# Kernel optimization log

Measured on AMD Instinct MI355X. Metric: run time of the kernel, lower is better.

The kernel has to match this reference:

```python
import jax, jax.numpy as jnp
import numpy as np

B, M, D, H, DH = 8, 1024, 768, 12, 64
R, RF, RW, DFF = 32, 384, 384, 3072
EPS = 1e-12  # BERT LayerNorm eps


def _ln(z, g, b):
    mu = jnp.mean(z, -1, keepdims=True)
    var = jnp.mean((z - mu) ** 2, -1, keepdims=True)
    return g * (z - mu) * jax.lax.rsqrt(var + EPS) + b


def setup_inputs() -> dict:
    ks = jax.random.split(jax.random.key(0), 20)
    n = lambda k, s: jax.random.normal(k, s, dtype=jnp.float32) * 0.02
    return {
        "x": jax.random.normal(ks[0], (B, M, D), dtype=jnp.float32),
        "mask": jnp.zeros((B, M), jnp.float32),  # additive attention mask
        "Pq": n(ks[1], (H, D, R)), "Vq": n(ks[2], (H, R, DH)), "bq": n(ks[3], (H, DH)),
        "Pk": n(ks[4], (H, D, R)), "Vk": n(ks[5], (H, R, DH)), "bk": n(ks[6], (H, DH)),
        "Pv": n(ks[7], (H, D, R)), "Vv": n(ks[8], (H, R, DH)), "bv": n(ks[9], (H, DH)),
        "Uo": n(ks[10], (D, RW)), "Vo": n(ks[11], (RW, D)), "bo_attn": n(ks[12], (D,)),
        "U1": n(ks[13], (D, RF)), "V1": n(ks[14], (RF, DFF)), "b1": n(ks[15], (DFF,)),
        "U2": n(ks[16], (DFF, RF)), "V2": n(ks[17], (RF, D)), "b2": n(ks[18], (D,)),
        "ln1_g": jnp.ones((D,), jnp.float32), "ln1_b": jnp.zeros((D,), jnp.float32),
        "ln2_g": jnp.ones((D,), jnp.float32), "ln2_b": jnp.zeros((D,), jnp.float32),
    }


def reference(x, mask, Pq, Vq, bq, Pk, Vk, bk, Pv, Vv, bv, Uo, Vo, bo_attn,
              U1, V1, b1, U2, V2, b2, ln1_g, ln1_b, ln2_g, ln2_b):
    Bx, Mx, dm = x.shape
    dh = dm // Pq.shape[0]
    scale = 1.0 / (dh ** 0.5)
    # low-rank per-head Q/K/V: x @ P (d->r) then @ V (r->dh), + per-head bias
    Q = jnp.einsum('bmd,hdr,hrk->bhmk', x, Pq, Vq) + bq[None, :, None, :]
    K = jnp.einsum('bmd,hdr,hrk->bhmk', x, Pk, Vk) + bk[None, :, None, :]
    V = jnp.einsum('bmd,hdr,hrk->bhmk', x, Pv, Vv) + bv[None, :, None, :]
    scores = jnp.einsum('bhmk,bhnk->bhmn', Q, K) * scale + mask[:, None, None, :]
    probs = jax.nn.softmax(scores, axis=-1)
    attn = jnp.einsum('bhmn,bhnk->bhmk', probs, V)
    attn = attn.transpose(0, 2, 1, 3).reshape(Bx, Mx, dm)  # (B, M, d_model)
    # low-rank attention output projection + residual + LN1
    x1 = _ln(x + (attn @ Uo) @ Vo + bo_attn, ln1_g, ln1_b)
    # low-rank FFN: GELU((x1 @ U1) @ V1 + b1) @ U2 @ V2 + b2 (BERT exact gelu)
    mid = x1 @ U1
    y = (jax.nn.gelu(mid @ V1 + b1, approximate=False) @ U2) @ V2 + b2
    return _ln(x1 + y, ln2_g, ln2_b)
```

## Files before the change

### kernel.cpp

```cpp
#include <hip/hip_runtime.h>
#include <cstddef>

#define D_MODEL 768
#define NHEAD   12
#define DHEAD   64
#define RANK    32
#define SEQ     1024
#define BATCH   8
#define BM      8192

typedef __attribute__((ext_vector_type(8))) short short8;
typedef __attribute__((ext_vector_type(4))) float floatx4;

__device__ inline ushort f2b(float f) {
  union { float f; unsigned u; } v; v.f = f;
  unsigned r = v.u + 0x7fffu + ((v.u >> 16) & 1u);
  return (ushort)(r >> 16);
}
__device__ inline float b2f(ushort h) {
  union { unsigned u; float f; } v; v.u = ((unsigned)h) << 16;
  return v.f;
}
__device__ inline unsigned pk2(float a, float b) {
  return ((__float_as_uint(b) + 0x8000u) & 0xffff0000u) |
         ((__float_as_uint(a) + 0x8000u) >> 16);
}
__device__ inline float fast_gelu(float x) {
  float z = 0.79788456080286536f * (x + 0.044715f * x * x * x);
  float e = __expf(2.f * z);
  float t = 1.f - 2.f / (e + 1.f);
  return 0.5f * x * (1.f + t);
}

__global__ __launch_bounds__(256) void f2b_kernel(
    const float* __restrict__ in, ushort* __restrict__ out, int n) {
  int i = (blockIdx.x * 256 + threadIdx.x) * 4;
  if (i >= n) return;
  float4 v = *(const float4*)(in + i);
  ushort4 o;
  o.x = f2b(v.x); o.y = f2b(v.y); o.z = f2b(v.z); o.w = f2b(v.w);
  *(ushort4*)(out + i) = o;
}

__global__ __launch_bounds__(256) void combine_qkv_kernel(
    const float* __restrict__ Pq, const float* __restrict__ Vq,
    const float* __restrict__ Pk, const float* __restrict__ Vk,
    const float* __restrict__ Pv, const float* __restrict__ Vv,
    ushort* __restrict__ Wt) {
  int which = blockIdx.y;
  const float* P  = which == 0 ? Pq : (which == 1 ? Pk : Pv);
  const float* Vw = which == 0 ? Vq : (which == 1 ? Vk : Vv);
  ushort* W = Wt + (size_t)which * D_MODEL * D_MODEL;
  int idx = blockIdx.x * 256 + threadIdx.x;
  if (idx >= D_MODEL * NHEAD * DHEAD) return;
  int c = idx / D_MODEL;
  int d = idx - c * D_MODEL;
  int h = c >> 6, k = c & 63;
  const float* p = P + ((size_t)h * D_MODEL + d) * RANK;
  const float* v = Vw + (size_t)h * RANK * DHEAD + k;
  float s = 0.f;
#pragma unroll
  for (int r = 0; r < RANK; r++) s += p[r] * v[(size_t)r * DHEAD];
  W[(size_t)c * D_MODEL + d] = f2b(s);
}

__global__ __launch_bounds__(256) void concat_bias_kernel(
    const float* __restrict__ bq, const float* __restrict__ bk,
    const float* __restrict__ bv, float* __restrict__ out) {
  int i = blockIdx.x * 256 + threadIdx.x;
  if (i >= 2304) return;
  out[i] = (i < 768) ? bq[i] : (i < 1536 ? bk[i - 768] : bv[i - 1536]);
}

__global__ __launch_bounds__(256) void prep_weights_kernel(
    const float* __restrict__ U1, const float* __restrict__ V1,
    const float* __restrict__ U2, const float* __restrict__ V2,
    const float* __restrict__ Vo, const float* __restrict__ Uo,
    ushort* __restrict__ U1t, ushort* __restrict__ V1t,
    ushort* __restrict__ U2t, ushort* __restrict__ V2t,
    ushort* __restrict__ VoT, ushort* __restrict__ Uob) {
  __shared__ float t[32][33];
  int blk = blockIdx.x;
  if (blk >= 3168) {
    int i = (blk - 3168) * 1024 + threadIdx.x * 4;
    float4 v = *(const float4*)(Uo + i);
    ushort4 o;
    o.x = f2b(v.x); o.y = f2b(v.y); o.z = f2b(v.z); o.w = f2b(v.w);
    *(ushort4*)(Uob + i) = o;
    return;
  }
  const float* in; ushort* out; int R, C, bx, by;
  if (blk < 288)       { in = U1; out = U1t; R = 768;  C = 384;  int i = blk;        bx = i % 12; by = i / 12; }
  else if (blk < 1440) { in = V1; out = V1t; R = 384;  C = 3072; int i = blk - 288;  bx = i % 96; by = i / 96; }
  else if (blk < 2592) { in = U2; out = U2t; R = 3072; C = 384;  int i = blk - 1440; bx = i % 12; by = i / 12; }
  else if (blk < 2880) { in = V2; out = V2t; R = 384;  C = 768;  int i = blk - 2592; bx = i % 24; by = i / 24; }
  else                 { in = Vo; out = VoT; R = 384;  C = 768;  int i = blk - 2880; bx = i % 24; by = i / 24; }
  int c0 = bx * 32, r0 = by * 32;
  int lx = threadIdx.x & 31, ly = threadIdx.x >> 5;
#pragma unroll
  for (int i = 0; i < 32; i += 8)
    t[ly + i][lx] = in[(size_t)(r0 + ly + i) * C + c0 + lx];
  __syncthreads();
#pragma unroll
  for (int i = 0; i < 32; i += 8)
    out[(size_t)(c0 + ly + i) * R + r0 + lx] = f2b(t[lx][ly + i]);
}

template <int OUTMODE, int BIAS, int GELU>
__global__ __launch_bounds__(256) void gemm_mfma_kernel(
    const ushort* __restrict__ A, const ushort* __restrict__ Bt,
    const float* __restrict__ bias, void* __restrict__ C,
    void* __restrict__ C2, void* __restrict__ C3,
    int M, int N, int K) {
  __shared__ __align__(16) ushort Als[128 * 32];
  __shared__ __align__(16) ushort Bls[128 * 32];
  const int tid  = threadIdx.x;
  const int lane = tid & 63;
  const int quad = lane >> 4, l16 = lane & 15;
  const int wu   = __builtin_amdgcn_readfirstlane(tid >> 6);
  const int wrow = (wu >> 1) * 64, wcol = (wu & 1) * 64;
  const int row0 = blockIdx.y * 128, col0 = blockIdx.x * 128;

  floatx4 acc[4][4] = {};

  for (int k0 = 0; k0 < K; k0 += 32) {
    __syncthreads();
#pragma unroll
    for (int is = 0; is < 2; is++) {
      int c = is * 256 + wu * 64 + lane;
      int m = c >> 2, kk = (c & 3) << 3;
      const ushort* ga = A + (size_t)(row0 + m) * K + (k0 + kk);
      ushort* la = Als + (size_t)(is * 256 + wu * 64) * 8;
      __builtin_amdgcn_global_load_lds(
          (const __attribute__((address_space(1))) void*)ga,
          (__attribute__((address_space(3))) void*)la, 16, 0, 0);
      const ushort* gb = Bt + (size_t)(col0 + m) * K + (k0 + kk);
      ushort* lb = Bls + (size_t)(is * 256 + wu * 64) * 8;
      __builtin_amdgcn_global_load_lds(
          (const __attribute__((address_space(1))) void*)gb,
          (__attribute__((address_space(3))) void*)lb, 16, 0, 0);
    }
    __syncthreads();

    short8 af[4], bf[4];
#pragma unroll
    for (int mt = 0; mt < 4; mt++)
      af[mt] = *(const short8*)(Als + ((wrow + mt * 16 + l16) * 32 + quad * 8));
#pragma unroll
    for (int nt = 0; nt < 4; nt++)
      bf[nt] = *(const short8*)(Bls + ((wcol + nt * 16 + l16) * 32 + quad * 8));
#pragma unroll
    for (int mt = 0; mt < 4; mt++)
#pragma unroll
      for (int nt = 0; nt < 4; nt++)
        acc[mt][nt] = __builtin_amdgcn_mfma_f32_16x16x32_bf16(
            af[mt], bf[nt], acc[mt][nt], 0, 0, 0);
  }

#pragma unroll
  for (int mt = 0; mt < 4; mt++) {
#pragma unroll
    for (int nt = 0; nt < 4; nt++) {
      int colg = col0 + wcol + nt * 16 + l16;
      float bv_ = BIAS ? bias[colg] : 0.f;
      float v4[4];
#pragma unroll
      for (int r = 0; r < 4; r++) {
        float v = acc[mt][nt][r] + bv_;
        if (GELU) v = fast_gelu(v);
        v4[r] = v;
      }
      int rowg0 = row0 + wrow + mt * 16 + quad * 4;
      if (OUTMODE == 3) {
        int seg = col0 / 768;
        int cl = colg - seg * 768;
        if (seg == 2) {
          ushort4 o;
          o.x = f2b(v4[0]); o.y = f2b(v4[1]); o.z = f2b(v4[2]); o.w = f2b(v4[3]);
          *(ushort4*)((ushort*)C3 + (size_t)cl * BM + rowg0) = o;
        } else {
          ushort* dst = (seg == 0) ? (ushort*)C : (ushort*)C2;
          float sc = (seg == 0) ? 0.125f : 1.f;
#pragma unroll
          for (int r = 0; r < 4; r++)
            dst[(size_t)(rowg0 + r) * D_MODEL + cl] = f2b(v4[r] * sc);
        }
      } else {
#pragma unroll
        for (int r = 0; r < 4; r++)
          ((ushort*)C)[(size_t)(rowg0 + r) * N + colg] = f2b(v4[r]);
      }
    }
  }
}

template <int BIAS>
__global__ __launch_bounds__(256) void gemm_n64_kernel(
    const ushort* __restrict__ A, const ushort* __restrict__ Bt,
    const float* __restrict__ bias, ushort* __restrict__ C,
    int M, int N, int K) {
  __shared__ __align__(16) ushort Als[128 * 32];
  __shared__ __align__(16) ushort Bls[64 * 32];
  const int tid  = threadIdx.x;
  const int lane = tid & 63;
  const int quad = lane >> 4, l16 = lane & 15;
  const int wu   = __builtin_amdgcn_readfirstlane(tid >> 6);
  const int row0 = blockIdx.y * 128, col0 = blockIdx.x * 64;

  floatx4 acc[2][4] = {};

  for (int k0 = 0; k0 < K; k0 += 32) {
    __syncthreads();
#pragma unroll
    for (int is = 0; is < 2; is++) {
      int c = is * 256 + wu * 64 + lane;
      int m = c >> 2, kk = (c & 3) << 3;
      const ushort* ga = A + (size_t)(row0 + m) * K + (k0 + kk);
      ushort* la = Als + (size_t)(is * 256 + wu * 64) * 8;
      __builtin_amdgcn_global_load_lds(
          (const __attribute__((address_space(1))) void*)ga,
          (__attribute__((address_space(3))) void*)la, 16, 0, 0);
    }
    {
      int c = wu * 64 + lane;
      int m = c >> 2, kk = (c & 3) << 3;
      const ushort* gb = Bt + (size_t)(col0 + m) * K + (k0 + kk);
      ushort* lb = Bls + (size_t)(wu * 64) * 8;
      __builtin_amdgcn_global_load_lds(
          (const __attribute__((address_space(1))) void*)gb,
          (__attribute__((address_space(3))) void*)lb, 16, 0, 0);
    }
    __syncthreads();

    short8 af[2], bf[4];
#pragma unroll
    for (int mt = 0; mt < 2; mt++)
      af[mt] = *(const short8*)(Als + ((wu * 32 + mt * 16 + l16) * 32 + quad * 8));
#pragma unroll
    for (int nt = 0; nt < 4; nt++)
      bf[nt] = *(const short8*)(Bls + ((nt * 16 + l16) * 32 + quad * 8));
#pragma unroll
    for (int mt = 0; mt < 2; mt++)
#pragma unroll
      for (int nt = 0; nt < 4; nt++)
        acc[mt][nt] = __builtin_amdgcn_mfma_f32_16x16x32_bf16(
            af[mt], bf[nt], acc[mt][nt], 0, 0, 0);
  }

#pragma unroll
  for (int mt = 0; mt < 2; mt++) {
#pragma unroll
    for (int nt = 0; nt < 4; nt++) {
      int colg = col0 + nt * 16 + l16;
      float bv_ = BIAS ? bias[colg] : 0.f;
      int rowg0 = row0 + wu * 32 + mt * 16 + quad * 4;
#pragma unroll
      for (int r = 0; r < 4; r++)
        C[(size_t)(rowg0 + r) * N + colg] = f2b(acc[mt][nt][r] + bv_);
    }
  }
}

__global__ __launch_bounds__(256) void gemm_mfma_splitk_kernel(
    const ushort* __restrict__ A, const ushort* __restrict__ Bt,
    float* __restrict__ Cpart, int M, int N, int Ktot, int Kper) {
  __shared__ __align__(16) ushort Als[128 * 32];
  __shared__ __align__(16) ushort Bls[128 * 32];
  const int tid  = threadIdx.x;
  const int lane = tid & 63;
  const int quad = lane >> 4, l16 = lane & 15;
  const int wu   = __builtin_amdgcn_readfirstlane(tid >> 6);
  const int wrow = (wu >> 1) * 64, wcol = (wu & 1) * 64;
  const int row0 = blockIdx.y * 128, col0 = blockIdx.x * 128;
  const int kbase = blockIdx.z * Kper;
  float* Cz = Cpart + (size_t)blockIdx.z * M * N;

  floatx4 acc[4][4] = {};

  for (int k0 = kbase; k0 < kbase + Kper; k0 += 32) {
    __syncthreads();
#pragma unroll
    for (int is = 0; is < 2; is++) {
      int c = is * 256 + wu * 64 + lane;
      int m = c >> 2, kk = (c & 3) << 3;
      const ushort* ga = A + (size_t)(row0 + m) * Ktot + (k0 + kk);
      ushort* la = Als + (size_t)(is * 256 + wu * 64) * 8;
      __builtin_amdgcn_global_load_lds(
          (const __attribute__((address_space(1))) void*)ga,
          (__attribute__((address_space(3))) void*)la, 16, 0, 0);
      const ushort* gb = Bt + (size_t)(col0 + m) * Ktot + (k0 + kk);
      ushort* lb = Bls + (size_t)(is * 256 + wu * 64) * 8;
      __builtin_amdgcn_global_load_lds(
          (const __attribute__((address_space(1))) void*)gb,
          (__attribute__((address_space(3))) void*)lb, 16, 0, 0);
    }
    __syncthreads();

    short8 af[4], bf[4];
#pragma unroll
    for (int mt = 0; mt < 4; mt++)
      af[mt] = *(const short8*)(Als + ((wrow + mt * 16 + l16) * 32 + quad * 8));
#pragma unroll
    for (int nt = 0; nt < 4; nt++)
      bf[nt] = *(const short8*)(Bls + ((wcol + nt * 16 + l16) * 32 + quad * 8));
#pragma unroll
    for (int mt = 0; mt < 4; mt++)
#pragma unroll
      for (int nt = 0; nt < 4; nt++)
        acc[mt][nt] = __builtin_amdgcn_mfma_f32_16x16x32_bf16(
            af[mt], bf[nt], acc[mt][nt], 0, 0, 0);
  }

#pragma unroll
  for (int mt = 0; mt < 4; mt++)
#pragma unroll
    for (int nt = 0; nt < 4; nt++) {
      int colg = col0 + wcol + nt * 16 + l16;
      int rowg0 = row0 + wrow + mt * 16 + quad * 4;
#pragma unroll
      for (int r = 0; r < 4; r++)
        Cz[(size_t)(rowg0 + r) * N + colg] = acc[mt][nt][r];
    }
}

__global__ __launch_bounds__(256) void reduce_splitk_kernel(
    const float* __restrict__ part, ushort* __restrict__ out, int n, int S) {
  int i = (blockIdx.x * 256 + threadIdx.x) * 4;
  if (i >= n) return;
  float4 a = *(const float4*)(part + i);
  for (int s = 1; s < S; s++) {
    float4 b = *(const float4*)(part + (size_t)s * n + i);
    a.x += b.x; a.y += b.y; a.z += b.z; a.w += b.w;
  }
  ushort4 o;
  o.x = f2b(a.x); o.y = f2b(a.y); o.z = f2b(a.z); o.w = f2b(a.w);
  *(ushort4*)(out + i) = o;
}

__global__ __launch_bounds__(256, 3) void attn_mfma_kernel(
    const ushort* __restrict__ Q, const ushort* __restrict__ K,
    const ushort* __restrict__ Vt, const float* __restrict__ mask,
    ushort* __restrict__ O) {
  const int bid  = blockIdx.x;
  const int xcd  = bid & 7;
  const int rest = bid >> 3;
  const int qt   = rest & 7;
  const int grp  = (rest >> 3) * 8 + xcd;
  const int h = grp % 12, b = grp / 12;

  const int tid = threadIdx.x;
  const int lane = tid & 63;
  const int quad = lane >> 4, l16 = lane & 15;
  const int wu = __builtin_amdgcn_readfirstlane(tid >> 6);
  const int qrow0 = qt * 128 + wu * 32;

  __shared__ __align__(16) ushort Ks[128 * 64];
  __shared__ __align__(16) ushort Vts[64 * 128];
  __shared__ __align__(16) float Msk[SEQ];

  *(float4*)(Msk + tid * 4) = *(const float4*)(mask + (size_t)b * SEQ + tid * 4);

  short8 qf[2][2];
#pragma unroll
  for (int rt = 0; rt < 2; rt++) {
    const ushort* qp = Q + ((size_t)(b * SEQ + qrow0 + rt * 16 + l16)) * D_MODEL
                     + h * DHEAD + quad * 8;
    qf[rt][0] = *(const short8*)qp;
    qf[rt][1] = *(const short8*)(qp + 32);
  }

  const int j0 = tid >> 3, ck = tid & 7;
  const int d0 = tid >> 4, cv = tid & 15;
  const ushort* Kg = K + ((size_t)(b * SEQ + j0)) * D_MODEL + h * DHEAD + ck * 8;
  const ushort* Vg = Vt + ((size_t)(h * DHEAD + d0)) * BM + b * SEQ + cv * 8;
  ushort* Kl = Ks + j0 * 64 + ((ck ^ (j0 & 7)) << 3);
  ushort* Vl = Vts + d0 * 128 + ((cv ^ (d0 & 15)) << 3);

  short8 kst[4], vst[4];
#pragma unroll
  for (int p = 0; p < 4; p++)
    kst[p] = *(const short8*)(Kg + (size_t)p * (32 * D_MODEL));
#pragma unroll
  for (int p = 0; p < 4; p++)
    vst[p] = *(const short8*)(Vg + (size_t)p * (16 * BM));

  float lsum[2] = {0.f, 0.f};
  floatx4 o_acc[2][4] = {};

  for (int n0 = 0; n0 < SEQ; n0 += 128) {
    asm volatile("" ::: "memory");
    __builtin_amdgcn_s_barrier();
    asm volatile("" ::: "memory");

#pragma unroll
    for (int p = 0; p < 4; p++) *(short8*)(Kl + p * (32 * 64)) = kst[p];
#pragma unroll
    for (int p = 0; p < 4; p++) *(short8*)(Vl + p * (16 * 128)) = vst[p];

    if (n0 + 128 < SEQ) {
#pragma unroll
      for (int p = 0; p < 4; p++)
        kst[p] = *(const short8*)(Kg + (size_t)(n0 + 128) * D_MODEL
                                     + (size_t)p * (32 * D_MODEL));
#pragma unroll
      for (int p = 0; p < 4; p++)
        vst[p] = *(const short8*)(Vg + (n0 + 128) + (size_t)p * (16 * BM));
    }

    asm volatile("s_waitcnt lgkmcnt(0)" ::: "memory");
    __builtin_amdgcn_s_barrier();
    asm volatile("" ::: "memory");

    unsigned UA[2][8], UB[2][8];
#pragma unroll
    for (int ct = 0; ct < 8; ct++) {
      int krow = ct * 16 + l16;
      int sa = (quad ^ (l16 & 7)) << 3;
      const ushort* kbp = Ks + krow * 64;
      short8 ka = *(const short8*)(kbp + sa);
      short8 kb = *(const short8*)(kbp + (sa ^ 32));
      float4 mk = *(const float4*)(Msk + n0 + ct * 16 + quad * 4);
#pragma unroll
      for (int rt = 0; rt < 2; rt++) {
        floatx4 st = {};
        st = __builtin_amdgcn_mfma_f32_16x16x32_bf16(ka, qf[rt][0], st, 0, 0, 0);
        st = __builtin_amdgcn_mfma_f32_16x16x32_bf16(kb, qf[rt][1], st, 0, 0, 0);
        float e0 = __expf(st[0] + mk.x);
        float e1 = __expf(st[1] + mk.y);
        float e2 = __expf(st[2] + mk.z);
        float e3 = __expf(st[3] + mk.w);
        lsum[rt] += (e0 + e1) + (e2 + e3);
        UA[rt][ct] = pk2(e0, e1);
        UB[rt][ct] = pk2(e2, e3);
      }
    }

#pragma unroll
    for (int kk = 0; kk < 4; kk++) {
      short8 pa[2];
#pragma unroll
      for (int rt = 0; rt < 2; rt++) {
        unsigned a0 = UA[rt][2 * kk], a2 = UA[rt][2 * kk + 1];
        unsigned b1 = UB[rt][2 * kk], b3 = UB[rt][2 * kk + 1];
        asm("v_permlane32_swap_b32 %0, %1" : "+v"(a0), "+v"(a2));
        asm("v_permlane16_swap_b32 %0, %1" : "+v"(a0), "+v"(a2));
        asm("v_permlane32_swap_b32 %0, %1" : "+v"(b1), "+v"(b3));
        asm("v_permlane16_swap_b32 %0, %1" : "+v"(b1), "+v"(b3));
        int4 t;
        t.x = (int)a0;
        t.y = (int)b1;
        t.z = (int)a2;
        t.w = (int)b3;
        pa[rt] = *(short8*)&t;
      }
#pragma unroll
      for (int dt = 0; dt < 4; dt++) {
        int vrow = dt * 16 + l16;
        short8 vb = *(const short8*)(Vts + vrow * 128
                                     + ((((kk * 4 + quad) ^ l16)) << 3));
#pragma unroll
        for (int rt = 0; rt < 2; rt++)
          o_acc[rt][dt] = __builtin_amdgcn_mfma_f32_16x16x32_bf16(pa[rt], vb, o_acc[rt][dt], 0, 0, 0);
      }
    }
  }

#pragma unroll
  for (int rt = 0; rt < 2; rt++) {
    float l = lsum[rt];
    l += __shfl_xor(l, 16);
    l += __shfl_xor(l, 32);
    float inv = 1.f / l;
    int lanebase = lane & 48;
#pragma unroll
    for (int rr = 0; rr < 4; rr++) {
      int iv = __builtin_amdgcn_ds_bpermute((lanebase | (quad * 4 + rr)) << 2,
                                            __float_as_int(inv));
      float invr = __int_as_float(iv);
      size_t rowg = (size_t)(b * SEQ + qrow0 + rt * 16 + quad * 4 + rr);
#pragma unroll
      for (int dt = 0; dt < 4; dt++)
        O[rowg * D_MODEL + h * DHEAD + dt * 16 + l16] = f2b(o_acc[rt][dt][rr] * invr);
    }
  }
}

template <int AIN_BF16, int OUT_FP32, int OUT_BF16>
__global__ __launch_bounds__(256) void add_ln_kernel(
    const float* __restrict__ Ainf, const ushort* __restrict__ Ainb,
    const ushort* __restrict__ Binb,
    const float* __restrict__ g, const float* __restrict__ bt,
    float* __restrict__ outf, ushort* __restrict__ outb) {
  const int row = blockIdx.x, tid = threadIdx.x;
  __shared__ float red[4];
  float v[3];
  float s = 0.f;
#pragma unroll
  for (int u = 0; u < 3; u++) {
    int c = tid + u * 256;
    float a = AIN_BF16 ? b2f(Ainb[(size_t)row * 768 + c]) : Ainf[(size_t)row * 768 + c];
    v[u] = a + b2f(Binb[(size_t)row * 768 + c]);
    s += v[u];
  }
#pragma unroll
  for (int off = 32; off > 0; off >>= 1) s += __shfl_down(s, off);
  if ((tid & 63) == 0) red[tid >> 6] = s;
  __syncthreads();
  float mu = (red[0] + red[1] + red[2] + red[3]) * (1.f / 768.f);
  float s2 = 0.f;
#pragma unroll
  for (int u = 0; u < 3; u++) { float d = v[u] - mu; s2 += d * d; }
#pragma unroll
  for (int off = 32; off > 0; off >>= 1) s2 += __shfl_down(s2, off);
  __syncthreads();
  if ((tid & 63) == 0) red[tid >> 6] = s2;
  __syncthreads();
  float var = (red[0] + red[1] + red[2] + red[3]) * (1.f / 768.f);
  float inv = rsqrtf(var + 1e-12f);
#pragma unroll
  for (int u = 0; u < 3; u++) {
    int c = tid + u * 256;
    float r = g[c] * (v[u] - mu) * inv + bt[c];
    if (OUT_FP32) outf[(size_t)row * 768 + c] = r;
    if (OUT_BF16) outb[(size_t)row * 768 + c] = f2b(r);
  }
}

extern "C" void kernel_launch(void* const* d_in, const int* in_sizes, int n_in,
                              void* d_out, int out_size, void* d_ws, size_t ws_size,
                              hipStream_t stream) {
  const float* x    = (const float*)d_in[0];
  const float* mask = (const float*)d_in[1];
  const float* Pq   = (const float*)d_in[2];
  const float* Vq   = (const float*)d_in[3];
  const float* bq   = (const float*)d_in[4];
  const float* Pk   = (const float*)d_in[5];
  const float* Vk   = (const float*)d_in[6];
  const float* bk   = (const float*)d_in[7];
  const float* Pv   = (const float*)d_in[8];
  const float* Vv   = (const float*)d_in[9];
  const float* bv   = (const float*)d_in[10];
  const float* Uo   = (const float*)d_in[11];
  const float* Vo   = (const float*)d_in[12];
  const float* bo   = (const float*)d_in[13];
  const float* U1   = (const float*)d_in[14];
  const float* V1   = (const float*)d_in[15];
  const float* b1   = (const float*)d_in[16];
  const float* U2   = (const float*)d_in[17];
  const float* V2   = (const float*)d_in[18];
  const float* b2   = (const float*)d_in[19];
  const float* g1   = (const float*)d_in[20];
  const float* be1  = (const float*)d_in[21];
  const float* g2   = (const float*)d_in[22];
  const float* be2  = (const float*)d_in[23];

  char* w = (char*)d_ws;
  auto alloc = [&](size_t bytes) -> char* {
    char* p = w; w += (bytes + 255) & ~(size_t)255; return p;
  };
  ushort* xb     = (ushort*)alloc((size_t)BM * 768 * 2);
  ushort* Wqkvt  = (ushort*)alloc((size_t)2304 * 768 * 2);
  float*  ball   = (float*)alloc(2304 * 4);
  ushort* VoT    = (ushort*)alloc(768 * 384 * 2);
  ushort* Uob    = (ushort*)alloc(768 * 384 * 2);
  ushort* Wot    = (ushort*)alloc(768 * 768 * 2);
  ushort* U1t    = (ushort*)alloc(384 * 768 * 2);
  ushort* V1t    = (ushort*)alloc((size_t)3072 * 384 * 2);
  ushort* U2t    = (ushort*)alloc((size_t)384 * 3072 * 2);
  ushort* V2t    = (ushort*)alloc(768 * 384 * 2);
  ushort* Qb     = (ushort*)alloc((size_t)BM * 768 * 2);
  ushort* Kb     = (ushort*)alloc((size_t)BM * 768 * 2);
  ushort* Vtb    = (ushort*)alloc((size_t)768 * BM * 2);
  ushort* attnb  = (ushort*)alloc((size_t)BM * 768 * 2);
  ushort* mtb    = (ushort*)alloc((size_t)BM * 384 * 2);
  ushort* y1b    = (ushort*)alloc((size_t)BM * 768 * 2);
  ushort* x1b    = (ushort*)alloc((size_t)BM * 768 * 2);
  float*  part   = (float*)alloc((size_t)4 * BM * 384 * 4);
  ushort* hiddenb = Qb;
  ushort* y2b     = y1b;
  float*  outp    = (float*)d_out;

  f2b_kernel<<<(BM * 768) / 1024, 256, 0, stream>>>(x, xb, BM * 768);
  combine_qkv_kernel<<<dim3(2304, 3), 256, 0, stream>>>(Pq, Vq, Pk, Vk, Pv, Vv, Wqkvt);
  concat_bias_kernel<<<9, 256, 0, stream>>>(bq, bk, bv, ball);
  prep_weights_kernel<<<3456, 256, 0, stream>>>(U1, V1, U2, V2, Vo, Uo,
                                                U1t, V1t, U2t, V2t, VoT, Uob);
  gemm_n64_kernel<0><<<dim3(12, 6), 256, 0, stream>>>(VoT, Uob, nullptr, Wot, 768, 768, 384);

  gemm_mfma_kernel<3, 1, 0><<<dim3(18, 64), 256, 0, stream>>>(
      xb, Wqkvt, ball, Qb, Kb, Vtb, BM, 2304, 768);

  attn_mfma_kernel<<<dim3(768), 256, 0, stream>>>(Qb, Kb, Vtb, mask, attnb);

  gemm_n64_kernel<1><<<dim3(12, 64), 256, 0, stream>>>(attnb, Wot, bo, y1b, BM, 768, 768);
  add_ln_kernel<0, 0, 1><<<BM, 256, 0, stream>>>(x, nullptr, y1b, g1, be1, nullptr, x1b);

  gemm_mfma_splitk_kernel<<<dim3(3, 64, 4), 256, 0, stream>>>(
      x1b, U1t, part, BM, 384, 768, 192);
  reduce_splitk_kernel<<<(BM * 384) / 1024, 256, 0, stream>>>(part, mtb, BM * 384, 4);
  gemm_mfma_kernel<1, 1, 1><<<dim3(24, 64), 256, 0, stream>>>(
      mtb, V1t, b1, hiddenb, nullptr, nullptr, BM, 3072, 384);
  gemm_mfma_splitk_kernel<<<dim3(3, 64, 4), 256, 0, stream>>>(
      hiddenb, U2t, part, BM, 384, 3072, 768);
  reduce_splitk_kernel<<<(BM * 384) / 1024, 256, 0, stream>>>(part, mtb, BM * 384, 4);
  gemm_n64_kernel<1><<<dim3(12, 64), 256, 0, stream>>>(mtb, V2t, b2, y2b, BM, 768, 384);

  add_ln_kernel<1, 1, 0><<<BM, 256, 0, stream>>>(nullptr, x1b, y2b, g2, be2, outp, nullptr);
}
```

Measured before the change: 461.0 us.

## Halve attention tile sizes to double grid and raise occupancy

The attention kernel now gives each block 64 query rows instead of 128, so each wave handles 16 rows, and streams K/V in 64-key chunks instead of 128. The grid doubles to 1536 blocks and launch bounds rise to 6 blocks per CU. Per-wave registers and LDS shrink, so more waves can hide latency. In exchange, K/V tiles are reloaded twice as often per query row, and there are more barriers per key processed.

```diff
diff --git a/kernel.cpp b/kernel.cpp
--- a/kernel.cpp
+++ b/kernel.cpp
@@ -337,137 +337,124 @@
   *(ushort4*)(out + i) = o;
 }
 
-__global__ __launch_bounds__(256, 3) void attn_mfma_kernel(
+__global__ __launch_bounds__(256, 6) void attn_mfma_kernel(
     const ushort* __restrict__ Q, const ushort* __restrict__ K,
     const ushort* __restrict__ Vt, const float* __restrict__ mask,
     ushort* __restrict__ O) {
   const int bid  = blockIdx.x;
   const int xcd  = bid & 7;
   const int rest = bid >> 3;
-  const int qt   = rest & 7;
-  const int grp  = (rest >> 3) * 8 + xcd;
+  const int qt   = rest & 15;
+  const int grp  = (rest >> 4) * 8 + xcd;
   const int h = grp % 12, b = grp / 12;
 
   const int tid = threadIdx.x;
   const int lane = tid & 63;
   const int quad = lane >> 4, l16 = lane & 15;
   const int wu = __builtin_amdgcn_readfirstlane(tid >> 6);
-  const int qrow0 = qt * 128 + wu * 32;
-
-  __shared__ __align__(16) ushort Ks[128 * 64];
-  __shared__ __align__(16) ushort Vts[64 * 128];
+  const int qrow0 = qt * 64 + wu * 16;
+
+  __shared__ __align__(16) ushort Ks[64 * 64];
+  __shared__ __align__(16) ushort Vts[64 * 64];
   __shared__ __align__(16) float Msk[SEQ];
 
   *(float4*)(Msk + tid * 4) = *(const float4*)(mask + (size_t)b * SEQ + tid * 4);
 
-  short8 qf[2][2];
-#pragma unroll
-  for (int rt = 0; rt < 2; rt++) {
-    const ushort* qp = Q + ((size_t)(b * SEQ + qrow0 + rt * 16 + l16)) * D_MODEL
+  short8 qf0, qf1;
+  {
+    const ushort* qp = Q + ((size_t)(b * SEQ + qrow0 + l16)) * D_MODEL
                      + h * DHEAD + quad * 8;
-    qf[rt][0] = *(const short8*)qp;
-    qf[rt][1] = *(const short8*)(qp + 32);
+    qf0 = *(const short8*)qp;
+    qf1 = *(const short8*)(qp + 32);
   }
 
   const int j0 = tid >> 3, ck = tid & 7;
-  const int d0 = tid >> 4, cv = tid & 15;
   const ushort* Kg = K + ((size_t)(b * SEQ + j0)) * D_MODEL + h * DHEAD + ck * 8;
-  const ushort* Vg = Vt + ((size_t)(h * DHEAD + d0)) * BM + b * SEQ + cv * 8;
+  const ushort* Vg = Vt + ((size_t)(h * DHEAD + j0)) * BM + b * SEQ + ck * 8;
   ushort* Kl = Ks + j0 * 64 + ((ck ^ (j0 & 7)) << 3);
-  ushort* Vl = Vts + d0 * 128 + ((cv ^ (d0 & 15)) << 3);
-
-  short8 kst[4], vst[4];
-#pragma unroll
-  for (int p = 0; p < 4; p++)
+  ushort* Vl = Vts + j0 * 64 + ((ck ^ (j0 & 7)) << 3);
+
+  short8 kst[2], vst[2];
+#pragma unroll
+  for (int p = 0; p < 2; p++)
     kst[p] = *(const short8*)(Kg + (size_t)p * (32 * D_MODEL));
 #pragma unroll
-  for (int p = 0; p < 4; p++)
-    vst[p] = *(const short8*)(Vg + (size_t)p * (16 * BM));
-
-  float lsum[2] = {0.f, 0.f};
-  floatx4 o_acc[2][4] = {};
-
-  for (int n0 = 0; n0 < SEQ; n0 += 128) {
+  for (int p = 0; p < 2; p++)
+    vst[p] = *(const short8*)(Vg + (size_t)p * (32 * BM));
+
+  float lsum = 0.f;
+  floatx4 o_acc[4] = {};
+
+  for (int n0 = 0; n0 < SEQ; n0 += 64) {
     asm volatile("" ::: "memory");
     __builtin_amdgcn_s_barrier();
     asm volatile("" ::: "memory");
 
 #pragma unroll
-    for (int p = 0; p < 4; p++) *(short8*)(Kl + p * (32 * 64)) = kst[p];
-#pragma unroll
-    for (int p = 0; p < 4; p++) *(short8*)(Vl + p * (16 * 128)) = vst[p];
-
-    if (n0 + 128 < SEQ) {
-#pragma unroll
-      for (int p = 0; p < 4; p++)
-        kst[p] = *(const short8*)(Kg + (size_t)(n0 + 128) * D_MODEL
-                                     + (size_t)p * (32 * D_MODEL));
-#pragma unroll
-      for (int p = 0; p < 4; p++)
-        vst[p] = *(const short8*)(Vg + (n0 + 128) + (size_t)p * (16 * BM));
+    for (int p = 0; p < 2; p++) *(short8*)(Kl + p * (32 * 64)) = kst[p];
+#pragma unroll
+    for (int p = 0; p < 2; p++) *(short8*)(Vl + p * (32 * 64)) = vst[p];
+
+    if (n0 + 64 < SEQ) {
+#pragma unroll
+      for (int p = 0; p < 2; p++)
+        kst[p] = *(const short8*)(Kg + (size_t)(n0 + 64 + p * 32) * D_MODEL);
+#pragma unroll
+      for (int p = 0; p < 2; p++)
+        vst[p] = *(const short8*)(Vg + (n0 + 64) + (size_t)p * (32 * BM));
     }
 
     asm volatile("s_waitcnt lgkmcnt(0)" ::: "memory");
     __builtin_amdgcn_s_barrier();
     asm volatile("" ::: "memory");
 
-    unsigned UA[2][8], UB[2][8];
-#pragma unroll
-    for (int ct = 0; ct < 8; ct++) {
+    unsigned UA[4], UB[4];
+#pragma unroll
+    for (int ct = 0; ct < 4; ct++) {
       int krow = ct * 16 + l16;
       int sa = (quad ^ (l16 & 7)) << 3;
       const ushort* kbp = Ks + krow * 64;
       short8 ka = *(const short8*)(kbp + sa);
       short8 kb = *(const short8*)(kbp + (sa ^ 32));
       float4 mk = *(const float4*)(Msk + n0 + ct * 16 + quad * 4);
-#pragma unroll
-      for (int rt = 0; rt < 2; rt++) {
-        floatx4 st = {};
-        st = __builtin_amdgcn_mfma_f32_16x16x32_bf16(ka, qf[rt][0], st, 0, 0, 0);
-        st = __builtin_amdgcn_mfma_f32_16x16x32_bf16(kb, qf[rt][1], st, 0, 0, 0);
-        float e0 = __expf(st[0] + mk.x);
-        float e1 = __expf(st[1] + mk.y);
-        float e2 = __expf(st[2] + mk.z);
-        float e3 = __expf(st[3] + mk.w);
-        lsum[rt] += (e0 + e1) + (e2 + e3);
-        UA[rt][ct] = pk2(e0, e1);
-        UB[rt][ct] = pk2(e2, e3);
+      floatx4 st = {};
+      st = __builtin_amdgcn_mfma_f32_16x16x32_bf16(ka, qf0, st, 0, 0, 0);
+      st = __builtin_amdgcn_mfma_f32_16x16x32_bf16(kb, qf1, st, 0, 0, 0);
+      float e0 = __expf(st[0] + mk.x);
+      float e1 = __expf(st[1] + mk.y);
+      float e2 = __expf(st[2] + mk.z);
+      float e3 = __expf(st[3] + mk.w);
+      lsum += (e0 + e1) + (e2 + e3);
+      UA[ct] = pk2(e0, e1);
+      UB[ct] = pk2(e2, e3);
+    }
+
+#pragma unroll
+    for (int kk = 0; kk < 2; kk++) {
+      unsigned a0 = UA[2 * kk], a2 = UA[2 * kk + 1];
+      unsigned b1 = UB[2 * kk], b3 = UB[2 * kk + 1];
+      asm("v_permlane32_swap_b32 %0, %1" : "+v"(a0), "+v"(a2));
+      asm("v_permlane16_swap_b32 %0, %1" : "+v"(a0), "+v"(a2));
+      asm("v_permlane32_swap_b32 %0, %1" : "+v"(b1), "+v"(b3));
+      asm("v_permlane16_swap_b32 %0, %1" : "+v"(b1), "+v"(b3));
+      int4 t;
+      t.x = (int)a0;
+      t.y = (int)b1;
+      t.z = (int)a2;
+      t.w = (int)b3;
+      short8 pa = *(short8*)&t;
+#pragma unroll
+      for (int dt = 0; dt < 4; dt++) {
+        int vr = dt * 16 + l16;
+        short8 vb = *(const short8*)(Vts + vr * 64
+                                     + (((kk * 4 + quad) ^ (l16 & 7)) << 3));
+        o_acc[dt] = __builtin_amdgcn_mfma_f32_16x16x32_bf16(pa, vb, o_acc[dt], 0, 0, 0);
       }
     }
-
-#pragma unroll
-    for (int kk = 0; kk < 4; kk++) {
-      short8 pa[2];
-#pragma unroll
-      for (int rt = 0; rt < 2; rt++) {
-        unsigned a0 = UA[rt][2 * kk], a2 = UA[rt][2 * kk + 1];
-        unsigned b1 = UB[rt][2 * kk], b3 = UB[rt][2 * kk + 1];
-        asm("v_permlane32_swap_b32 %0, %1" : "+v"(a0), "+v"(a2));
-        asm("v_permlane16_swap_b32 %0, %1" : "+v"(a0), "+v"(a2));
-        asm("v_permlane32_swap_b32 %0, %1" : "+v"(b1), "+v"(b3));
-        asm("v_permlane16_swap_b32 %0, %1" : "+v"(b1), "+v"(b3));
-        int4 t;
-        t.x = (int)a0;
-        t.y = (int)b1;
-        t.z = (int)a2;
-        t.w = (int)b3;
-        pa[rt] = *(short8*)&t;
-      }
-#pragma unroll
-      for (int dt = 0; dt < 4; dt++) {
-        int vrow = dt * 16 + l16;
-        short8 vb = *(const short8*)(Vts + vrow * 128
-                                     + ((((kk * 4 + quad) ^ l16)) << 3));
-#pragma unroll
-        for (int rt = 0; rt < 2; rt++)
-          o_acc[rt][dt] = __builtin_amdgcn_mfma_f32_16x16x32_bf16(pa[rt], vb, o_acc[rt][dt], 0, 0, 0);
-      }
-    }
-  }
-
-#pragma unroll
-  for (int rt = 0; rt < 2; rt++) {
-    float l = lsum[rt];
+  }
+
+  {
+    float l = lsum;
     l += __shfl_xor(l, 16);
     l += __shfl_xor(l, 32);
     float inv = 1.f / l;
@@ -477,10 +464,10 @@
       int iv = __builtin_amdgcn_ds_bpermute((lanebase | (quad * 4 + rr)) << 2,
                                             __float_as_int(inv));
       float invr = __int_as_float(iv);
-      size_t rowg = (size_t)(b * SEQ + qrow0 + rt * 16 + quad * 4 + rr);
+      size_t rowg = (size_t)(b * SEQ + qrow0 + quad * 4 + rr);
 #pragma unroll
       for (int dt = 0; dt < 4; dt++)
-        O[rowg * D_MODEL + h * DHEAD + dt * 16 + l16] = f2b(o_acc[rt][dt][rr] * invr);
+        O[rowg * D_MODEL + h * DHEAD + dt * 16 + l16] = f2b(o_acc[dt][rr] * invr);
     }
   }
 }
@@ -590,7 +577,7 @@
   gemm_mfma_kernel<3, 1, 0><<<dim3(18, 64), 256, 0, stream>>>(
       xb, Wqkvt, ball, Qb, Kb, Vtb, BM, 2304, 768);
 
-  attn_mfma_kernel<<<dim3(768), 256, 0, stream>>>(Qb, Kb, Vtb, mask, attnb);
+  attn_mfma_kernel<<<dim3(1536), 256, 0, stream>>>(Qb, Kb, Vtb, mask, attnb);
 
   gemm_n64_kernel<1><<<dim3(12, 64), 256, 0, stream>>>(attnb, Wot, bo, y1b, BM, 768, 768);
   add_ln_kernel<0, 0, 1><<<BM, 256, 0, stream>>>(x, nullptr, y1b, g1, be1, nullptr, x1b);
```

Result: slower. 473.8 us (+2.8%).

## Double-buffer K/V tiles in LDS with 64-key steps in attention kernel

Applied to the files above, without the earlier changes.

Restructures the attention inner loop so K and V^T tiles are staged through two 64-key LDS buffers. The next tile is written while the current one is computed, which leaves one barrier per iteration instead of two. It also raises wave priority around the MFMA section with s_setprio. The cost is twice as many loop iterations with smaller MFMA batches per barrier, plus a changed V swizzle pattern that has to stay bank-conflict free.

```diff
diff --git a/kernel.cpp b/kernel.cpp
--- a/kernel.cpp
+++ b/kernel.cpp
@@ -354,8 +354,8 @@
   const int wu = __builtin_amdgcn_readfirstlane(tid >> 6);
   const int qrow0 = qt * 128 + wu * 32;
 
-  __shared__ __align__(16) ushort Ks[128 * 64];
-  __shared__ __align__(16) ushort Vts[64 * 128];
+  __shared__ __align__(16) ushort Ks[2][64 * 64];
+  __shared__ __align__(16) ushort Vts[2][64 * 64];
   __shared__ __align__(16) float Msk[SEQ];
 
   *(float4*)(Msk + tid * 4) = *(const float4*)(mask + (size_t)b * SEQ + tid * 4);
@@ -370,53 +370,58 @@
   }
 
   const int j0 = tid >> 3, ck = tid & 7;
-  const int d0 = tid >> 4, cv = tid & 15;
   const ushort* Kg = K + ((size_t)(b * SEQ + j0)) * D_MODEL + h * DHEAD + ck * 8;
-  const ushort* Vg = Vt + ((size_t)(h * DHEAD + d0)) * BM + b * SEQ + cv * 8;
-  ushort* Kl = Ks + j0 * 64 + ((ck ^ (j0 & 7)) << 3);
-  ushort* Vl = Vts + d0 * 128 + ((cv ^ (d0 & 15)) << 3);
-
-  short8 kst[4], vst[4];
-#pragma unroll
-  for (int p = 0; p < 4; p++)
-    kst[p] = *(const short8*)(Kg + (size_t)p * (32 * D_MODEL));
-#pragma unroll
-  for (int p = 0; p < 4; p++)
-    vst[p] = *(const short8*)(Vg + (size_t)p * (16 * BM));
+  const ushort* Vg = Vt + ((size_t)(h * DHEAD + j0)) * BM + b * SEQ + ck * 8;
+  const int kloff = j0 * 64 + ((ck ^ (j0 & 7)) << 3);
+
+  short8 kst[2], vst[2];
+#pragma unroll
+  for (int p = 0; p < 2; p++) {
+    kst[p] = *(const short8*)(Kg + (size_t)(p * 32) * D_MODEL);
+    vst[p] = *(const short8*)(Vg + (size_t)p * (32 * BM));
+  }
+#pragma unroll
+  for (int p = 0; p < 2; p++) {
+    *(short8*)(&Ks[0][0] + kloff + p * (32 * 64)) = kst[p];
+    *(short8*)(&Vts[0][0] + kloff + p * (32 * 64)) = vst[p];
+  }
+#pragma unroll
+  for (int p = 0; p < 2; p++) {
+    kst[p] = *(const short8*)(Kg + (size_t)(64 + p * 32) * D_MODEL);
+    vst[p] = *(const short8*)(Vg + 64 + (size_t)p * (32 * BM));
+  }
+  asm volatile("s_waitcnt lgkmcnt(0)" ::: "memory");
+  __builtin_amdgcn_s_barrier();
+  asm volatile("" ::: "memory");
 
   float lsum[2] = {0.f, 0.f};
   floatx4 o_acc[2][4] = {};
 
-  for (int n0 = 0; n0 < SEQ; n0 += 128) {
-    asm volatile("" ::: "memory");
-    __builtin_amdgcn_s_barrier();
-    asm volatile("" ::: "memory");
-
-#pragma unroll
-    for (int p = 0; p < 4; p++) *(short8*)(Kl + p * (32 * 64)) = kst[p];
-#pragma unroll
-    for (int p = 0; p < 4; p++) *(short8*)(Vl + p * (16 * 128)) = vst[p];
-
-    if (n0 + 128 < SEQ) {
-#pragma unroll
-      for (int p = 0; p < 4; p++)
-        kst[p] = *(const short8*)(Kg + (size_t)(n0 + 128) * D_MODEL
-                                     + (size_t)p * (32 * D_MODEL));
-#pragma unroll
-      for (int p = 0; p < 4; p++)
-        vst[p] = *(const short8*)(Vg + (n0 + 128) + (size_t)p * (16 * BM));
-    }
-
-    asm volatile("s_waitcnt lgkmcnt(0)" ::: "memory");
-    __builtin_amdgcn_s_barrier();
-    asm volatile("" ::: "memory");
-
-    unsigned UA[2][8], UB[2][8];
-#pragma unroll
-    for (int ct = 0; ct < 8; ct++) {
+  for (int n0 = 0; n0 < SEQ; n0 += 64) {
+    const int cur = (n0 >> 6) & 1;
+
+    if (n0 + 64 < SEQ) {
+#pragma unroll
+      for (int p = 0; p < 2; p++) {
+        *(short8*)(&Ks[cur ^ 1][0] + kloff + p * (32 * 64)) = kst[p];
+        *(short8*)(&Vts[cur ^ 1][0] + kloff + p * (32 * 64)) = vst[p];
+      }
+      if (n0 + 128 < SEQ) {
+#pragma unroll
+        for (int p = 0; p < 2; p++) {
+          kst[p] = *(const short8*)(Kg + (size_t)(n0 + 128 + p * 32) * D_MODEL);
+          vst[p] = *(const short8*)(Vg + (n0 + 128) + (size_t)p * (32 * BM));
+        }
+      }
+    }
+
+    __builtin_amdgcn_s_setprio(1);
+    unsigned UA[2][4], UB[2][4];
+#pragma unroll
+    for (int ct = 0; ct < 4; ct++) {
       int krow = ct * 16 + l16;
       int sa = (quad ^ (l16 & 7)) << 3;
-      const ushort* kbp = Ks + krow * 64;
+      const ushort* kbp = &Ks[cur][0] + krow * 64;
       short8 ka = *(const short8*)(kbp + sa);
       short8 kb = *(const short8*)(kbp + (sa ^ 32));
       float4 mk = *(const float4*)(Msk + n0 + ct * 16 + quad * 4);
@@ -436,7 +441,7 @@
     }
 
 #pragma unroll
-    for (int kk = 0; kk < 4; kk++) {
+    for (int kk = 0; kk < 2; kk++) {
       short8 pa[2];
 #pragma unroll
       for (int rt = 0; rt < 2; rt++) {
@@ -455,13 +460,21 @@
       }
 #pragma unroll
       for (int dt = 0; dt < 4; dt++) {
-        int vrow = dt * 16 + l16;
-        short8 vb = *(const short8*)(Vts + vrow * 128
-                                     + ((((kk * 4 + quad) ^ l16)) << 3));
+        int vr = dt * 16 + l16;
+        short8 vb = *(const short8*)(&Vts[cur][0] + vr * 64
+                                     + (((kk * 4 + quad) ^ (l16 & 7)) << 3));
 #pragma unroll
         for (int rt = 0; rt < 2; rt++)
-          o_acc[rt][dt] = __builtin_amdgcn_mfma_f32_16x16x32_bf16(pa[rt], vb, o_acc[rt][dt], 0, 0, 0);
+          o_acc[rt][dt] = __builtin_amdgcn_mfma_f32_16x16x32_bf16(
+              pa[rt], vb, o_acc[rt][dt], 0, 0, 0);
       }
+    }
+    __builtin_amdgcn_s_setprio(0);
+
+    if (n0 + 64 < SEQ) {
+      asm volatile("s_waitcnt lgkmcnt(0)" ::: "memory");
+      __builtin_amdgcn_s_barrier();
+      asm volatile("" ::: "memory");
     }
   }
 
```

Measured after the change: 436.2 us. 5.4% less time.
